# Kernel optimization log

Hardware: AMD Instinct MI355X
Metric: run time of the kernel (lower is better)

Reference implementation:

```python
import jax, jax.numpy as jnp
import numpy as np
import math

N_HEADS = 16  # from init_kwargs

def setup_inputs() -> dict:
    key = jax.random.key(0)
    ks = jax.random.split(key, 8)
    B, S, D = 2, 2048, 1024
    dk = D // N_HEADS
    # rotary frequencies: theta_i = 10000^(-2i/dk), angles = pos * theta
    inv_freq = 1.0 / (10000.0 ** (jnp.arange(0, dk, 2, dtype=jnp.float32) / dk))
    angles = jnp.arange(S, dtype=jnp.float32)[:, None] * inv_freq[None, :]  # [S, dk/2]
    scale = 0.02
    return {
        "x": jax.random.normal(ks[0], (B, S, D), dtype=jnp.float32),
        "freq_cos": jnp.cos(angles),
        "freq_sin": jnp.sin(angles),
        "Wq": jax.random.normal(ks[1], (D, D), dtype=jnp.float32) * scale,
        "Wk": jax.random.normal(ks[2], (D, D), dtype=jnp.float32) * scale,
        "Wv": jax.random.normal(ks[3], (D, D), dtype=jnp.float32) * scale,
        "Wo": jax.random.normal(ks[4], (D, D), dtype=jnp.float32) * scale,
    }

def _apply_rope(t, freq_cos, freq_sin):
    # t: [B, S, H, dk]; interpret last dim as dk/2 complex pairs (even=real, odd=imag)
    B, S, H, dk = t.shape
    tr = t.reshape(B, S, H, dk // 2, 2)
    re, im = tr[..., 0], tr[..., 1]
    c = freq_cos[None, :, None, :]  # [1, S, 1, dk/2]
    s = freq_sin[None, :, None, :]
    out_re = re * c - im * s
    out_im = re * s + im * c
    return jnp.stack([out_re, out_im], axis=-1).reshape(B, S, H, dk)

def reference(x, freq_cos, freq_sin, Wq, Wk, Wv, Wo):
    B, S, D = x.shape
    H = N_HEADS
    dk = D // H
    q = (x @ Wq).reshape(B, S, H, dk)
    k = (x @ Wk).reshape(B, S, H, dk)
    v = (x @ Wv).reshape(B, S, H, dk)
    q = _apply_rope(q, freq_cos, freq_sin)
    k = _apply_rope(k, freq_cos, freq_sin)
    # [B, H, S, dk]
    q = q.transpose(0, 2, 1, 3)
    k = k.transpose(0, 2, 1, 3)
    v = v.transpose(0, 2, 1, 3)
    scores = jnp.einsum('bhqd,bhkd->bhqk', q, k) / math.sqrt(dk)
    # faithful to source: softmax applied TWICE
    p = jax.nn.softmax(scores, axis=-1)
    p = jax.nn.softmax(p, axis=-1)
    out = jnp.einsum('bhqk,bhkd->bhqd', p, v)
    out = out.transpose(0, 2, 1, 3).reshape(B, S, D)
    return out @ Wo
```

## Files before the change

kernel.cpp:

```cpp
#include <hip/hip_runtime.h>
#include <cstdint>

typedef unsigned short u16;
typedef unsigned int u32;
typedef __attribute__((ext_vector_type(8))) short bf16x8;
typedef __attribute__((ext_vector_type(4))) short bf16x4;
typedef __attribute__((ext_vector_type(4))) float f32x4;

__device__ __forceinline__ float bf2f(short h) {
  union { u32 u; float f; } x; x.u = ((u32)(u16)h) << 16; return x.f;
}
__device__ __forceinline__ short f2bf(float f) {
  union { float f; u32 u; } x; x.f = f;
  u32 r = x.u + 0x7fffu + ((x.u >> 16) & 1u);
  return (short)(u16)(r >> 16);
}

__device__ __forceinline__ void gload16(const void* g, void* l) {
  __builtin_amdgcn_global_load_lds(
      (const __attribute__((address_space(1))) u32*)g,
      (__attribute__((address_space(3))) u32*)l, 16, 0, 0);
}

__global__ __launch_bounds__(256) void cast_k(const float* __restrict__ in,
                                              u16* __restrict__ out) {
  int i = blockIdx.x * 256 + threadIdx.x;
  const float4* p = (const float4*)(in + (size_t)i * 8);
  float4 a = p[0], b = p[1];
  bf16x8 v;
  v[0] = f2bf(a.x); v[1] = f2bf(a.y); v[2] = f2bf(a.z); v[3] = f2bf(a.w);
  v[4] = f2bf(b.x); v[5] = f2bf(b.y); v[6] = f2bf(b.z); v[7] = f2bf(b.w);
  *(bf16x8*)(out + (size_t)i * 8) = v;
}

__global__ __launch_bounds__(256) void castT4_k(
    const float* __restrict__ W0, const float* __restrict__ W1,
    const float* __restrict__ W2, const float* __restrict__ W3,
    u16* __restrict__ O0, u16* __restrict__ O1,
    u16* __restrict__ O2, u16* __restrict__ O3) {
  __shared__ u16 Ts[64 * 72];
  const int z = blockIdx.z;
  const float* in = z == 0 ? W0 : (z == 1 ? W1 : (z == 2 ? W2 : W3));
  u16* out = z == 0 ? O0 : (z == 1 ? O1 : (z == 2 ? O2 : O3));
  const int k0 = blockIdx.x * 64, n0 = blockIdx.y * 64;
  const int t = threadIdx.x;
  const int kr = t >> 4, nc = (t & 15) * 4;
#pragma unroll
  for (int p = 0; p < 4; ++p) {
    float4 v = *(const float4*)(in + (size_t)(k0 + kr + p * 16) * 1024 + n0 + nc);
    int kk = kr + p * 16;
    Ts[(nc + 0) * 72 + kk] = (u16)f2bf(v.x);
    Ts[(nc + 1) * 72 + kk] = (u16)f2bf(v.y);
    Ts[(nc + 2) * 72 + kk] = (u16)f2bf(v.z);
    Ts[(nc + 3) * 72 + kk] = (u16)f2bf(v.w);
  }
  __syncthreads();
  const int nr = t >> 2, kc = (t & 3) * 16;
  bf16x8 o0, o1;
#pragma unroll
  for (int j = 0; j < 8; ++j) {
    o0[j] = (short)Ts[nr * 72 + kc + j];
    o1[j] = (short)Ts[nr * 72 + kc + 8 + j];
  }
  *(bf16x8*)(out + (size_t)(n0 + nr) * 1024 + k0 + kc) = o0;
  *(bf16x8*)(out + (size_t)(n0 + nr) * 1024 + k0 + kc + 8) = o1;
}

template <int NJ>
__device__ __forceinline__ void gemm_core(char* gsm, const u16* __restrict__ A,
                                          const u16* __restrict__ Bt,
                                          int row0, int col0,
                                          f32x4 (&acc)[4][NJ]) {
  constexpr int SB = 16384 + NJ * 4096;
  const int t = threadIdx.x;
  const int l = t & 63, w = t >> 6;
  const int lq = l & 15, g = l >> 4;
  const int wr = w >> 1, wc = w & 1;
  const int r8 = t >> 3;
  const int c8 = (((t & 7) ^ (r8 & 7)) << 3);

  auto stage = [&](int cb, int k0) {
    char* dst = gsm + cb * SB + w * 1024;
#pragma unroll
    for (int p = 0; p < 4; ++p)
      gload16(A + (size_t)(row0 + r8 + 32 * p) * 1024 + k0 + c8, dst + p * 4096);
#pragma unroll
    for (int p = 0; p < NJ; ++p)
      gload16(Bt + (size_t)(col0 + r8 + 32 * p) * 1024 + k0 + c8,
              dst + 16384 + p * 4096);
  };

  stage(0, 0);
  __syncthreads();
  int cur = 0;
  for (int k0 = 0; k0 < 1024; k0 += 64) {
    if (k0 + 64 < 1024) stage(cur ^ 1, k0 + 64);
    const char* Ab = gsm + cur * SB;
#pragma unroll
    for (int ks = 0; ks < 2; ++ks) {
      bf16x8 af[4], bfr[NJ];
      const int sA = ks * 4 + g;
#pragma unroll
      for (int i = 0; i < 4; ++i) {
        int ra = wr * 64 + i * 16 + lq;
        af[i] = *(const bf16x8*)(Ab + ra * 128 + ((sA ^ (ra & 7)) << 4));
      }
#pragma unroll
      for (int j = 0; j < NJ; ++j) {
        int rb = wc * (NJ * 16) + j * 16 + lq;
        bfr[j] = *(const bf16x8*)(Ab + 16384 + rb * 128 + ((sA ^ (rb & 7)) << 4));
      }
#pragma unroll
      for (int i = 0; i < 4; ++i)
#pragma unroll
        for (int j = 0; j < NJ; ++j)
          acc[i][j] = __builtin_amdgcn_mfma_f32_16x16x32_bf16(af[i], bfr[j],
                                                              acc[i][j], 0, 0, 0);
    }
    __syncthreads();
    cur ^= 1;
  }
}

__global__ __launch_bounds__(256) void gemm_qkv_k(
    const u16* __restrict__ xb, const u16* __restrict__ Wqt,
    const u16* __restrict__ Wkt, const u16* __restrict__ Wvt,
    u16* __restrict__ Qb, u16* __restrict__ Kb, u16* __restrict__ Vr,
    const float* __restrict__ cosT, const float* __restrict__ sinT) {
  __shared__ __align__(16) char gsm[65536];
  const int which = blockIdx.y >> 3;
  const u16* Bt = which == 0 ? Wqt : (which == 1 ? Wkt : Wvt);
  const int row0 = blockIdx.x * 128, col0 = (blockIdx.y & 7) * 128;

  f32x4 acc[4][4] = {};
  gemm_core<4>(gsm, xb, Bt, row0, col0, acc);

  const int t = threadIdx.x;
  const int l = t & 63, w = t >> 6;
  const int lq = l & 15, g = l >> 4;
  const int wr = w >> 1, wc = w & 1;
  const float SC = 0.18033688011112042f;

  if (which == 2) {
#pragma unroll
    for (int i = 0; i < 4; ++i)
#pragma unroll
      for (int j = 0; j < 4; ++j)
#pragma unroll
        for (int jr = 0; jr < 4; ++jr) {
          int row = row0 + wr * 64 + i * 16 + 4 * g + jr;
          int col = col0 + wc * 64 + j * 16 + lq;
          Vr[(size_t)row * 1024 + col] = (u16)f2bf(acc[i][j][jr]);
        }
  } else {
    u16* dstB = which == 0 ? Qb : Kb;
    const float sc = which == 0 ? SC : 1.0f;
#pragma unroll
    for (int i = 0; i < 4; ++i)
#pragma unroll
      for (int j = 0; j < 4; ++j)
#pragma unroll
        for (int jr = 0; jr < 4; ++jr) {
          int row = row0 + wr * 64 + i * 16 + 4 * g + jr;
          int col = col0 + wc * 64 + j * 16 + lq;
          int bb = row >> 11, ss = row & 2047;
          int hh = col >> 6, dd = col & 63;
          float v = acc[i][j][jr];
          float pv = __shfl_xor(v, 1);
          float c = cosT[ss * 32 + (dd >> 1)];
          float s = sinT[ss * 32 + (dd >> 1)];
          float o = (dd & 1) ? (pv * s + v * c) : (v * c - pv * s);
          dstB[(((size_t)bb * 16 + hh) * 2048 + ss) * 64 + dd] = (u16)f2bf(o * sc);
        }
  }
}

__global__ __launch_bounds__(256) void gemm_o_k(const u16* __restrict__ A,
                                                const u16* __restrict__ Bt,
                                                float* __restrict__ C) {
  __shared__ __align__(16) char gsm[49152];
  const int row0 = blockIdx.x * 128, col0 = blockIdx.y * 64;
  f32x4 acc[4][2] = {};
  gemm_core<2>(gsm, A, Bt, row0, col0, acc);
  const int t = threadIdx.x;
  const int l = t & 63, w = t >> 6;
  const int lq = l & 15, g = l >> 4;
  const int wr = w >> 1, wc = w & 1;
#pragma unroll
  for (int i = 0; i < 4; ++i)
#pragma unroll
    for (int j = 0; j < 2; ++j)
#pragma unroll
      for (int jr = 0; jr < 4; ++jr) {
        int row = row0 + wr * 64 + i * 16 + 4 * g + jr;
        int col = col0 + wc * 32 + j * 16 + lq;
        C[(size_t)row * 1024 + col] = acc[i][j][jr];
      }
}

__global__ __launch_bounds__(256) void transV_k(const u16* __restrict__ Vr,
                                                u16* __restrict__ Vt,
                                                float* __restrict__ sumVp) {
  __shared__ u16 Ls[64 * 72];
  __shared__ float Sbuf[4][64];
  const int bh = blockIdx.y, s0 = blockIdx.x * 64;
  const int b = bh >> 4, h = bh & 15;
  const int t = threadIdx.x;
  const int sr = t >> 3, su = t & 7;
#pragma unroll
  for (int p = 0; p < 2; ++p) {
    int srow = sr + p * 32;
    bf16x8 v = *(const bf16x8*)(Vr + (size_t)(b * 2048 + s0 + srow) * 1024 + h * 64 + su * 8);
    *(bf16x8*)((char*)Ls + (srow * 72 + su * 8) * 2) = v;
  }
  __syncthreads();
  const int d = t >> 2, sc = (t & 3) * 16;
  const int base = (sc & 32) + ((sc >> 4) & 1) * 4;
  u16* dst = Vt + ((size_t)bh * 64 + d) * 2048 + s0 + base;
#pragma unroll
  for (int q = 0; q < 4; ++q) {
    bf16x4 c;
#pragma unroll
    for (int jj = 0; jj < 4; ++jj) c[jj] = (short)Ls[(sc + q * 4 + jj) * 72 + d];
    *(bf16x4*)(dst + 8 * q) = c;
  }
  const int d2 = t & 63, seg = t >> 6;
  float part = 0.f;
#pragma unroll
  for (int rr = 0; rr < 16; ++rr) part += bf2f((short)Ls[(seg * 16 + rr) * 72 + d2]);
  Sbuf[seg][d2] = part;
  __syncthreads();
  if (t < 64)
    sumVp[((size_t)blockIdx.x * 32 + bh) * 64 + t] =
        Sbuf[0][t] + Sbuf[1][t] + Sbuf[2][t] + Sbuf[3][t];
}

__global__ __launch_bounds__(256) void attn_k(const u16* __restrict__ Qb,
                                              const u16* __restrict__ Kb,
                                              const u16* __restrict__ Vt,
                                              const float* __restrict__ sumVp,
                                              u16* __restrict__ Cb) {
  __shared__ __align__(16) char smem[33280];
  float* Lbuf = (float*)(smem + 32768);
  const int t = threadIdx.x;
  const int l = t & 63, w = t >> 6;
  const int lq = l & 15, g = l >> 4;
  const int qh = w & 1, kh = w >> 1;
  const int bid = blockIdx.y * 64 + blockIdx.x;
  const int wg = (bid & 7) * 256 + (bid >> 3);
  const int bh = wg >> 6, q0 = (wg & 63) * 32;
  const int b = bh >> 4, h = bh & 15;

  const int sQ = q0 + qh * 16 + lq;
  const u16* qr = Qb + ((size_t)bh * 2048 + sQ) * 64;
  const bf16x8 qf0 = *(const bf16x8*)(qr + g * 8);
  const bf16x8 qf1 = *(const bf16x8*)(qr + 32 + g * 8);

  const int r8 = t >> 3;
  const int c8 = (((t & 7) ^ (r8 & 7)) << 3);
  const size_t kbase = (size_t)bh * 2048 * 64;
  const size_t vbase = (size_t)bh * 64 * 2048;

  auto stage = [&](int cb, int j0) {
    char* dst = smem + cb * 16384 + w * 1024;
#pragma unroll
    for (int p = 0; p < 2; ++p) {
      gload16(Kb + kbase + (size_t)(j0 + r8 + 32 * p) * 64 + c8, dst + p * 4096);
      gload16(Vt + vbase + (size_t)(r8 + 32 * p) * 2048 + j0 + c8,
              dst + 8192 + p * 4096);
    }
  };

  float l1 = 0.0f;
  f32x4 accO[4] = {};

  stage(0, 0);
  __syncthreads();
  int cur = 0;
  for (int j0 = 0; j0 < 2048; j0 += 64) {
    if (j0 + 64 < 2048) stage(cur ^ 1, j0 + 64);
    const char* Kl = smem + cur * 16384;
    const char* Vl = Kl + 8192;
    f32x4 sc[2] = {};
#pragma unroll
    for (int ks = 0; ks < 2; ++ks)
#pragma unroll
      for (int kt = 0; kt < 2; ++kt) {
        int r = kh * 32 + kt * 16 + lq, sA = ks * 4 + g;
        bf16x8 af = *(const bf16x8*)(Kl + r * 128 + ((sA ^ (r & 7)) << 4));
        sc[kt] = __builtin_amdgcn_mfma_f32_16x16x32_bf16(af, ks ? qf1 : qf0,
                                                         sc[kt], 0, 0, 0);
      }
    float wv[2][4];
#pragma unroll
    for (int kt = 0; kt < 2; ++kt)
#pragma unroll
      for (int jr = 0; jr < 4; ++jr) {
        float e;
        asm("v_exp_f32 %0, %1" : "=v"(e) : "v"(sc[kt][jr]));
        wv[kt][jr] = e;
        l1 += e;
      }
    union { bf16x8 v; u32 uw[4]; } pb;
    asm("v_cvt_pk_bf16_f32 %0, %1, %2" : "=v"(pb.uw[0]) : "v"(wv[0][0]), "v"(wv[0][1]));
    asm("v_cvt_pk_bf16_f32 %0, %1, %2" : "=v"(pb.uw[1]) : "v"(wv[0][2]), "v"(wv[0][3]));
    asm("v_cvt_pk_bf16_f32 %0, %1, %2" : "=v"(pb.uw[2]) : "v"(wv[1][0]), "v"(wv[1][1]));
    asm("v_cvt_pk_bf16_f32 %0, %1, %2" : "=v"(pb.uw[3]) : "v"(wv[1][2]), "v"(wv[1][3]));
#pragma unroll
    for (int dt = 0; dt < 4; ++dt) {
      int dd = dt * 16 + lq;
      bf16x8 av = *(const bf16x8*)(Vl + dd * 128 +
                                   (((kh * 4 + g) ^ (dd & 7)) << 4));
      accO[dt] = __builtin_amdgcn_mfma_f32_16x16x32_bf16(av, pb.v, accO[dt], 0, 0, 0);
    }
    __syncthreads();
    cur ^= 1;
  }

  l1 += __shfl_xor(l1, 16);
  l1 += __shfl_xor(l1, 32);
  if (l < 16) Lbuf[w * 16 + l] = l1;
  __syncthreads();
  const float l1tot = Lbuf[w * 16 + lq] + Lbuf[(w ^ 2) * 16 + lq];
  const float rl1 = 1.0f / l1tot;

  float* Tb = (float*)smem;
  if (kh == 0) {
#pragma unroll
    for (int dt = 0; dt < 4; ++dt)
#pragma unroll
      for (int jr = 0; jr < 4; ++jr)
        Tb[(qh * 16 + lq) * 65 + dt * 16 + 4 * g + jr] = accO[dt][jr];
    if (l < 16) Lbuf[64 + qh * 16 + l] = rl1;
  }
  __syncthreads();
  if (kh == 1) {
#pragma unroll
    for (int dt = 0; dt < 4; ++dt)
#pragma unroll
      for (int jr = 0; jr < 4; ++jr)
        Tb[(qh * 16 + lq) * 65 + dt * 16 + 4 * g + jr] += accO[dt][jr];
  }
  __syncthreads();
  const int qq = t >> 3, dc = (t & 7) * 8;
  const float rq = Lbuf[64 + qq];
  f32x4 s0 = {}, s1 = {};
#pragma unroll 8
  for (int sl = 0; sl < 32; ++sl) {
    s0 += *(const f32x4*)(sumVp + ((size_t)sl * 32 + bh) * 64 + dc);
    s1 += *(const f32x4*)(sumVp + ((size_t)sl * 32 + bh) * 64 + dc + 4);
  }
  const float inv2049 = 1.0f / 2049.0f;
  bf16x8 o;
#pragma unroll
  for (int j = 0; j < 4; ++j) {
    o[j]     = f2bf((Tb[qq * 65 + dc + j] * rq + s0[j]) * inv2049);
    o[4 + j] = f2bf((Tb[qq * 65 + dc + 4 + j] * rq + s1[j]) * inv2049);
  }
  size_t obase = ((size_t)(b * 2048 + q0 + qq)) * 1024 + h * 64 + dc;
  *(bf16x8*)(Cb + obase) = o;
}

extern "C" void kernel_launch(void* const* d_in, const int* in_sizes, int n_in,
                              void* d_out, int out_size, void* d_ws, size_t ws_size,
                              hipStream_t stream) {
  const float* x = (const float*)d_in[0];
  const float* fcos = (const float*)d_in[1];
  const float* fsin = (const float*)d_in[2];
  const float* Wq = (const float*)d_in[3];
  const float* Wk = (const float*)d_in[4];
  const float* Wv = (const float*)d_in[5];
  const float* Wo = (const float*)d_in[6];
  float* out = (float*)d_out;

  char* wsp = (char*)d_ws;
  u16* xb  = (u16*)(wsp);
  u16* Wqt = (u16*)(wsp + (8ull << 20));
  u16* Wkt = (u16*)(wsp + (10ull << 20));
  u16* Wvt = (u16*)(wsp + (12ull << 20));
  u16* Wot = (u16*)(wsp + (14ull << 20));
  u16* Qb  = (u16*)(wsp + (16ull << 20));
  u16* Kb  = (u16*)(wsp + (24ull << 20));
  u16* Vr  = (u16*)(wsp + (32ull << 20));
  u16* Vt  = (u16*)(wsp + (40ull << 20));
  u16* Cb  = (u16*)(wsp + (48ull << 20));
  float* sumVp = (float*)(wsp + (8ull << 20));

  cast_k<<<2048, 256, 0, stream>>>(x, xb);
  dim3 gT(16, 16, 4);
  castT4_k<<<gT, 256, 0, stream>>>(Wq, Wk, Wv, Wo, Wqt, Wkt, Wvt, Wot);

  dim3 gQKV(32, 24);
  gemm_qkv_k<<<gQKV, 256, 0, stream>>>(xb, Wqt, Wkt, Wvt, Qb, Kb, Vr,
                                       fcos, fsin);

  dim3 gV(32, 32);
  transV_k<<<gV, 256, 0, stream>>>(Vr, Vt, sumVp);

  dim3 gA(64, 32);
  attn_k<<<gA, 256, 0, stream>>>(Qb, Kb, Vt, sumVp, Cb);

  dim3 gO(32, 16);
  gemm_o_k<<<gO, 256, 0, stream>>>(Cb, Wot, out);
}
```

Baseline: 208.1 us.

## Give each attention wave its own query rows over the full key tile

Each attention block now covers 64 queries, with every wave owning 16 queries and processing all 64 keys per tile, where before the key dimension was split across wave pairs. This removes the cross-wave reduction of partial outputs and row sums through shared memory, and halves the grid so each K/V tile is loaded once for twice as many queries. The per-head sum of V is reduced once at kernel start and overlapped with the first tile load, and the XCD-aware block remapping is dropped. In exchange each wave issues twice the MFMAs per tile, needs more registers, and the grid has fewer blocks to spread across CUs.

```diff
diff --git a/kernel.cpp b/kernel.cpp
--- a/kernel.cpp
+++ b/kernel.cpp
@@ -241,17 +241,14 @@
                                               const float* __restrict__ sumVp,
                                               u16* __restrict__ Cb) {
   __shared__ __align__(16) char smem[33280];
-  float* Lbuf = (float*)(smem + 32768);
+  float* Svb = (float*)(smem + 32768);
   const int t = threadIdx.x;
   const int l = t & 63, w = t >> 6;
   const int lq = l & 15, g = l >> 4;
-  const int qh = w & 1, kh = w >> 1;
-  const int bid = blockIdx.y * 64 + blockIdx.x;
-  const int wg = (bid & 7) * 256 + (bid >> 3);
-  const int bh = wg >> 6, q0 = (wg & 63) * 32;
+  const int bh = blockIdx.y, q0 = blockIdx.x * 64;
   const int b = bh >> 4, h = bh & 15;
 
-  const int sQ = q0 + qh * 16 + lq;
+  const int sQ = q0 + w * 16 + lq;
   const u16* qr = Qb + ((size_t)bh * 2048 + sQ) * 64;
   const bf16x8 qf0 = *(const bf16x8*)(qr + g * 8);
   const bf16x8 qf1 = *(const bf16x8*)(qr + 32 + g * 8);
@@ -271,29 +268,35 @@
     }
   };
 
+  stage(0, 0);
+  if (t < 64) {
+    float sv = 0.f;
+#pragma unroll 8
+    for (int sl = 0; sl < 32; ++sl) sv += sumVp[((size_t)sl * 32 + bh) * 64 + t];
+    Svb[t] = sv;
+  }
+  __syncthreads();
+
   float l1 = 0.0f;
   f32x4 accO[4] = {};
-
-  stage(0, 0);
-  __syncthreads();
   int cur = 0;
   for (int j0 = 0; j0 < 2048; j0 += 64) {
     if (j0 + 64 < 2048) stage(cur ^ 1, j0 + 64);
     const char* Kl = smem + cur * 16384;
     const char* Vl = Kl + 8192;
-    f32x4 sc[2] = {};
+    f32x4 sc[4] = {};
 #pragma unroll
     for (int ks = 0; ks < 2; ++ks)
 #pragma unroll
-      for (int kt = 0; kt < 2; ++kt) {
-        int r = kh * 32 + kt * 16 + lq, sA = ks * 4 + g;
+      for (int kt = 0; kt < 4; ++kt) {
+        int r = kt * 16 + lq, sA = ks * 4 + g;
         bf16x8 af = *(const bf16x8*)(Kl + r * 128 + ((sA ^ (r & 7)) << 4));
         sc[kt] = __builtin_amdgcn_mfma_f32_16x16x32_bf16(af, ks ? qf1 : qf0,
                                                          sc[kt], 0, 0, 0);
       }
-    float wv[2][4];
-#pragma unroll
-    for (int kt = 0; kt < 2; ++kt)
+    float wv[4][4];
+#pragma unroll
+    for (int kt = 0; kt < 4; ++kt)
 #pragma unroll
       for (int jr = 0; jr < 4; ++jr) {
         float e;
@@ -301,17 +304,22 @@
         wv[kt][jr] = e;
         l1 += e;
       }
-    union { bf16x8 v; u32 uw[4]; } pb;
-    asm("v_cvt_pk_bf16_f32 %0, %1, %2" : "=v"(pb.uw[0]) : "v"(wv[0][0]), "v"(wv[0][1]));
-    asm("v_cvt_pk_bf16_f32 %0, %1, %2" : "=v"(pb.uw[1]) : "v"(wv[0][2]), "v"(wv[0][3]));
-    asm("v_cvt_pk_bf16_f32 %0, %1, %2" : "=v"(pb.uw[2]) : "v"(wv[1][0]), "v"(wv[1][1]));
-    asm("v_cvt_pk_bf16_f32 %0, %1, %2" : "=v"(pb.uw[3]) : "v"(wv[1][2]), "v"(wv[1][3]));
+    union { bf16x8 v; u32 uw[4]; } pbA, pbB;
+    asm("v_cvt_pk_bf16_f32 %0, %1, %2" : "=v"(pbA.uw[0]) : "v"(wv[0][0]), "v"(wv[0][1]));
+    asm("v_cvt_pk_bf16_f32 %0, %1, %2" : "=v"(pbA.uw[1]) : "v"(wv[0][2]), "v"(wv[0][3]));
+    asm("v_cvt_pk_bf16_f32 %0, %1, %2" : "=v"(pbA.uw[2]) : "v"(wv[1][0]), "v"(wv[1][1]));
+    asm("v_cvt_pk_bf16_f32 %0, %1, %2" : "=v"(pbA.uw[3]) : "v"(wv[1][2]), "v"(wv[1][3]));
+    asm("v_cvt_pk_bf16_f32 %0, %1, %2" : "=v"(pbB.uw[0]) : "v"(wv[2][0]), "v"(wv[2][1]));
+    asm("v_cvt_pk_bf16_f32 %0, %1, %2" : "=v"(pbB.uw[1]) : "v"(wv[2][2]), "v"(wv[2][3]));
+    asm("v_cvt_pk_bf16_f32 %0, %1, %2" : "=v"(pbB.uw[2]) : "v"(wv[3][0]), "v"(wv[3][1]));
+    asm("v_cvt_pk_bf16_f32 %0, %1, %2" : "=v"(pbB.uw[3]) : "v"(wv[3][2]), "v"(wv[3][3]));
 #pragma unroll
     for (int dt = 0; dt < 4; ++dt) {
       int dd = dt * 16 + lq;
-      bf16x8 av = *(const bf16x8*)(Vl + dd * 128 +
-                                   (((kh * 4 + g) ^ (dd & 7)) << 4));
-      accO[dt] = __builtin_amdgcn_mfma_f32_16x16x32_bf16(av, pb.v, accO[dt], 0, 0, 0);
+      bf16x8 avA = *(const bf16x8*)(Vl + dd * 128 + ((g ^ (dd & 7)) << 4));
+      accO[dt] = __builtin_amdgcn_mfma_f32_16x16x32_bf16(avA, pbA.v, accO[dt], 0, 0, 0);
+      bf16x8 avB = *(const bf16x8*)(Vl + dd * 128 + (((4 + g) ^ (dd & 7)) << 4));
+      accO[dt] = __builtin_amdgcn_mfma_f32_16x16x32_bf16(avB, pbB.v, accO[dt], 0, 0, 0);
     }
     __syncthreads();
     cur ^= 1;
@@ -319,46 +327,26 @@
 
   l1 += __shfl_xor(l1, 16);
   l1 += __shfl_xor(l1, 32);
-  if (l < 16) Lbuf[w * 16 + l] = l1;
-  __syncthreads();
-  const float l1tot = Lbuf[w * 16 + lq] + Lbuf[(w ^ 2) * 16 + lq];
-  const float rl1 = 1.0f / l1tot;
+  const float rl1 = 1.0f / l1;
 
   float* Tb = (float*)smem;
-  if (kh == 0) {
-#pragma unroll
-    for (int dt = 0; dt < 4; ++dt)
-#pragma unroll
-      for (int jr = 0; jr < 4; ++jr)
-        Tb[(qh * 16 + lq) * 65 + dt * 16 + 4 * g + jr] = accO[dt][jr];
-    if (l < 16) Lbuf[64 + qh * 16 + l] = rl1;
-  }
-  __syncthreads();
-  if (kh == 1) {
-#pragma unroll
-    for (int dt = 0; dt < 4; ++dt)
-#pragma unroll
-      for (int jr = 0; jr < 4; ++jr)
-        Tb[(qh * 16 + lq) * 65 + dt * 16 + 4 * g + jr] += accO[dt][jr];
-  }
-  __syncthreads();
-  const int qq = t >> 3, dc = (t & 7) * 8;
-  const float rq = Lbuf[64 + qq];
-  f32x4 s0 = {}, s1 = {};
-#pragma unroll 8
-  for (int sl = 0; sl < 32; ++sl) {
-    s0 += *(const f32x4*)(sumVp + ((size_t)sl * 32 + bh) * 64 + dc);
-    s1 += *(const f32x4*)(sumVp + ((size_t)sl * 32 + bh) * 64 + dc + 4);
-  }
+#pragma unroll
+  for (int dt = 0; dt < 4; ++dt)
+#pragma unroll
+    for (int jr = 0; jr < 4; ++jr)
+      Tb[(w * 16 + lq) * 65 + dt * 16 + 4 * g + jr] = accO[dt][jr] * rl1;
+  __syncthreads();
+  const int qq = t >> 2, dc = (t & 3) * 16;
   const float inv2049 = 1.0f / 2049.0f;
-  bf16x8 o;
-#pragma unroll
-  for (int j = 0; j < 4; ++j) {
-    o[j]     = f2bf((Tb[qq * 65 + dc + j] * rq + s0[j]) * inv2049);
-    o[4 + j] = f2bf((Tb[qq * 65 + dc + 4 + j] * rq + s1[j]) * inv2049);
+  bf16x8 o0, o1;
+#pragma unroll
+  for (int j = 0; j < 8; ++j) {
+    o0[j] = f2bf((Tb[qq * 65 + dc + j] + Svb[dc + j]) * inv2049);
+    o1[j] = f2bf((Tb[qq * 65 + dc + 8 + j] + Svb[dc + 8 + j]) * inv2049);
   }
   size_t obase = ((size_t)(b * 2048 + q0 + qq)) * 1024 + h * 64 + dc;
-  *(bf16x8*)(Cb + obase) = o;
+  *(bf16x8*)(Cb + obase) = o0;
+  *(bf16x8*)(Cb + obase + 8) = o1;
 }
 
 extern "C" void kernel_launch(void* const* d_in, const int* in_sizes, int n_in,
@@ -397,7 +385,7 @@
   dim3 gV(32, 32);
   transV_k<<<gV, 256, 0, stream>>>(Vr, Vt, sumVp);
 
-  dim3 gA(64, 32);
+  dim3 gA(32, 32);
   attn_k<<<gA, 256, 0, stream>>>(Qb, Kb, Vt, sumVp, Cb);
 
   dim3 gO(32, 16);
```

After: 188.7 us. -9.3%, faster.
